# Optimization experiments

Measured on AMD Instinct MI355X. Metric: run time of the kernel, lower is better.

Reference implementation:

```python
import jax, jax.numpy as jnp
import numpy as np

B, F, H, D, TE, CE = 16384, 1024, 64, 256, 4, 4

def setup_inputs() -> dict:
    key = jax.random.key(0)
    ks = iter(jax.random.split(key, 40))
    s = 0.02
    mk = lambda shape: jax.random.normal(next(ks), shape, jnp.float32) * s
    inp = {
        'x_A': jax.random.normal(next(ks), (B, F), jnp.float32),
        'x_S': jax.random.normal(next(ks), (B, F), jnp.float32),
        'x_B': jax.random.normal(next(ks), (B, F), jnp.float32),
        # stacked per-expert weights for the three expert groups (A, Shared, B)
        'W1A': mk((TE, F, H)), 'b1A': mk((TE, H)), 'W2A': mk((TE, H, D)), 'b2A': mk((TE, D)),
        'W1S': mk((CE, F, H)), 'b1S': mk((CE, H)), 'W2S': mk((CE, H, D)), 'b2S': mk((CE, D)),
        'W1B': mk((TE, F, H)), 'b1B': mk((TE, H)), 'W2B': mk((TE, H, D)), 'b2B': mk((TE, D)),
        # gate weights
        'WgA': mk((F, TE + CE)), 'bgA': mk((TE + CE,)),
        'WgB': mk((F, TE + CE)), 'bgB': mk((TE + CE,)),
        'WgS': mk((F, 2 * TE + CE)), 'bgS': mk((2 * TE + CE,)),
    }
    return inp

def _expert_group(x, W1, b1, W2, b2):
    # x: [B,F], W1: [E,F,H] -> [B,E,H]; W2: [E,H,D] -> [B,E,D]
    h = jax.nn.relu(jnp.einsum('bf,efh->beh', x, W1) + b1)  # dropout p=0 -> identity
    return jax.nn.relu(jnp.einsum('beh,ehd->bed', h, W2) + b2)

def reference(x_A, x_S, x_B,
              W1A, b1A, W2A, b2A,
              W1S, b1S, W2S, b2S,
              W1B, b1B, W2B, b2B,
              WgA, bgA, WgB, bgB, WgS, bgS):
    EA = _expert_group(x_A, W1A, b1A, W2A, b2A)  # [B,TE,D]
    ES = _expert_group(x_S, W1S, b1S, W2S, b2S)  # [B,CE,D]
    EB = _expert_group(x_B, W1B, b1B, W2B, b2B)  # [B,TE,D]
    gA = jax.nn.softmax(x_A @ WgA + bgA, axis=1)  # [B,TE+CE]
    gS = jax.nn.softmax(x_S @ WgS + bgS, axis=1)  # [B,2TE+CE]
    gB = jax.nn.softmax(x_B @ WgB + bgB, axis=1)  # [B,TE+CE]
    outA = jnp.einsum('bed,be->bd', jnp.concatenate([EA, ES], axis=1), gA)
    outS = jnp.einsum('bed,be->bd', jnp.concatenate([EA, ES, EB], axis=1), gS)
    outB = jnp.einsum('bed,be->bd', jnp.concatenate([EB, ES], axis=1), gB)
    return (outA, outS, outB)
```

## Files before the change

### kernel.cpp

```cpp
#include <hip/hip_runtime.h>


#define BB 16384
#define FF 1024

typedef _Float16 f16;
typedef __fp16 h16x2 __attribute__((ext_vector_type(2)));
typedef _Float16 f16x8 __attribute__((ext_vector_type(8)));
typedef float f32x4 __attribute__((ext_vector_type(4)));

__device__ __forceinline__ void load_lds16(const void* g, void* l) {
    __builtin_amdgcn_global_load_lds(
        (const __attribute__((address_space(1))) unsigned int*)g,
        (__attribute__((address_space(3))) unsigned int*)l, 16, 0, 0);
}

__device__ __forceinline__ f16x8 pack8(float4 lo, float4 hi) {
    union { f16x8 v; h16x2 p[4]; } u;
    u.p[0] = __builtin_amdgcn_cvt_pkrtz(lo.x, lo.y);
    u.p[1] = __builtin_amdgcn_cvt_pkrtz(lo.z, lo.w);
    u.p[2] = __builtin_amdgcn_cvt_pkrtz(hi.x, hi.y);
    u.p[3] = __builtin_amdgcn_cvt_pkrtz(hi.z, hi.w);
    return u.v;
}

__global__ __launch_bounds__(256) void pack_kernel(
    const float* __restrict__ W1A, const float* __restrict__ W1S, const float* __restrict__ W1B,
    const float* __restrict__ W2A, const float* __restrict__ W2S, const float* __restrict__ W2B,
    const float* __restrict__ WgA, const float* __restrict__ WgS, const float* __restrict__ WgB,
    f16* __restrict__ Wp, f16* __restrict__ W2T, f16* __restrict__ Gp)
{
    int idx = blockIdx.x * 256 + threadIdx.x;
    if (idx < 786432) {
        int g = idx / 262144, rem = idx % 262144;
        int c = rem >> 10, k = rem & 1023;
        const float* W1 = (g == 0) ? W1A : ((g == 1) ? W1S : W1B);
        Wp[idx] = (f16)W1[((c >> 6) << 16) + k * 64 + (c & 63)];
    } else if (idx < 983040) {
        int j = idx - 786432;
        int g = j / 65536, rem = j % 65536;
        int e = rem >> 14, rr = rem & 16383;
        int d = rr >> 6, hh = rr & 63;
        const float* W2 = (g == 0) ? W2A : ((g == 1) ? W2S : W2B);
        W2T[j] = (f16)W2[e * 16384 + hh * 256 + d];
    } else {
        int j = idx - 983040;
        int g = j / 16384, rem = j % 16384;
        int k = rem >> 4, c = rem & 15;
        int ng = (g == 1) ? 12 : 8;
        const float* Wg = (g == 0) ? WgA : ((g == 1) ? WgS : WgB);
        Gp[j] = (c < ng) ? (f16)Wg[k * ng + c] : (f16)0.0f;
    }
}

__global__ __launch_bounds__(256) void l1_kernel(
    const float* __restrict__ xA, const float* __restrict__ xS, const float* __restrict__ xB,
    const float* __restrict__ b1A, const float* __restrict__ b1S, const float* __restrict__ b1B,
    const float* __restrict__ bgA, const float* __restrict__ bgS, const float* __restrict__ bgB,
    const f16* __restrict__ Wp,
    const f16* __restrict__ Gp,
    f16* __restrict__ hbuf,
    float* __restrict__ gates)
{
    const int g = blockIdx.z;
    const float* x  = (g == 0) ? xA  : ((g == 1) ? xS  : xB);
    const float* b1 = (g == 0) ? b1A : ((g == 1) ? b1S : b1B);
    const float* bg = (g == 0) ? bgA : ((g == 1) ? bgS : bgB);
    const int ng = (g == 1) ? 12 : 8;
    float* gout = gates + ((g == 0) ? (size_t)0
                         : (g == 1) ? (size_t)BB * 8
                                    : (size_t)BB * 8 + (size_t)BB * 12);

    const int row0 = blockIdx.y * 128;
    const int col0 = blockIdx.x * 128;
    const bool do_gate = (blockIdx.x == 0);

    __shared__ __align__(16) float Asf[128 * 32];
    __shared__ __align__(16) f16   Bsh[128 * 32];
    __shared__ __align__(16) f16   Gs[16 * 40];

    const int tid  = threadIdx.x;
    const int lane = tid & 63;
    const int wave = tid >> 6;
    const int wm = (wave >> 1) * 64;
    const int wn = (wave & 1) * 64;
    const int lrow = lane & 15;
    const int quad = lane >> 4;

    const f16* Wgrp = Wp + (size_t)g * 256 * 1024;
    const f16* Ggrp = Gp + (size_t)g * 1024 * 16;

    f32x4 acc[4][4] = {};
    f32x4 gacc[4] = {};
    const bool my_gate = do_gate && ((wave & 1) == 0);

    for (int k0 = 0; k0 < FF; k0 += 32) {
#pragma unroll
        for (int r = 0; r < 4; ++r) {
            int s = r * 256 + tid;
            int m = s >> 3, slot = s & 7;
            int seg = slot ^ (m & 7);
            load_lds16(x + (size_t)(row0 + m) * FF + k0 + seg * 4, Asf + s * 4);
        }
#pragma unroll
        for (int r = 0; r < 2; ++r) {
            int s = r * 256 + tid;
            int m = s >> 2, slot = s & 3;
            int seg = slot ^ ((m >> 1) & 3);
            load_lds16(Wgrp + (size_t)(col0 + m) * FF + k0 + seg * 8, Bsh + s * 8);
        }
        if (do_gate) {
#pragma unroll
            for (int r = 0; r < 2; ++r) {
                int idx = r * 256 + tid;
                int k = idx >> 4, c = idx & 15;
                Gs[c * 40 + k] = Ggrp[(size_t)(k0 + k) * 16 + c];
            }
        }
        __syncthreads();

        f16x8 af[4], bfr[4];
#pragma unroll
        for (int i = 0; i < 4; ++i) {
            int m = wm + i * 16 + lrow;
            const float* rp = Asf + m * 32;
            int s0 = (2 * quad) ^ (m & 7);
            int s1 = s0 ^ 1;
            float4 lo = *(const float4*)(rp + s0 * 4);
            float4 hi = *(const float4*)(rp + s1 * 4);
            af[i] = pack8(lo, hi);
        }
#pragma unroll
        for (int j = 0; j < 4; ++j) {
            int n = wn + j * 16 + lrow;
            int slot = quad ^ ((n >> 1) & 3);
            bfr[j] = *(const f16x8*)(Bsh + n * 32 + slot * 8);
        }
#pragma unroll
        for (int i = 0; i < 4; ++i)
#pragma unroll
            for (int j = 0; j < 4; ++j)
                acc[i][j] = __builtin_amdgcn_mfma_f32_16x16x32_f16(af[i], bfr[j], acc[i][j], 0, 0, 0);
        if (my_gate) {
            f16x8 gb = *(const f16x8*)(Gs + lrow * 40 + quad * 8);
#pragma unroll
            for (int i = 0; i < 4; ++i)
                gacc[i] = __builtin_amdgcn_mfma_f32_16x16x32_f16(af[i], gb, gacc[i], 0, 0, 0);
        }
        __syncthreads();
    }

#pragma unroll
    for (int j = 0; j < 4; ++j) {
        int c = col0 + wn + j * 16 + lrow;
        float bias = b1[c];
#pragma unroll
        for (int i = 0; i < 4; ++i) {
#pragma unroll
            for (int r = 0; r < 4; ++r) {
                int row = row0 + wm + i * 16 + quad * 4 + r;
                float v = fmaxf(acc[i][j][r] + bias, 0.0f);
                hbuf[((size_t)g * BB + row) * 256 + c] = (f16)v;
            }
        }
    }

    if (my_gate) {
        int c = lrow;
        bool valid = (c < ng);
        float bias = valid ? bg[c] : 0.0f;
#pragma unroll
        for (int i = 0; i < 4; ++i) {
#pragma unroll
            for (int r = 0; r < 4; ++r) {
                int row = row0 + wm + i * 16 + quad * 4 + r;
                float logit = valid ? (gacc[i][r] + bias) : -1e30f;
                float mx = logit;
#pragma unroll
                for (int m = 1; m < 16; m <<= 1)
                    mx = fmaxf(mx, __shfl_xor(mx, m, 16));
                float ev = valid ? __expf(logit - mx) : 0.0f;
                float sum = ev;
#pragma unroll
                for (int m = 1; m < 16; m <<= 1)
                    sum += __shfl_xor(sum, m, 16);
                if (valid) gout[(size_t)row * ng + c] = ev / sum;
            }
        }
    }
}

__global__ __launch_bounds__(256) void l2_kernel(
    const f16* __restrict__ hbuf,
    const f16* __restrict__ W2T,
    const float* __restrict__ b2A, const float* __restrict__ b2S, const float* __restrict__ b2B,
    const float* __restrict__ gates,
    float* __restrict__ out)
{
    const int o = blockIdx.y;
    const int row0 = blockIdx.x * 64;
    const int tid = threadIdx.x;
    const int lane = tid & 63;
    const int wave = tid >> 6;
    const int wn = wave * 64;
    const int lrow = lane & 15;
    const int quad = lane >> 4;

    const int ng = (o == 1) ? 12 : 8;
    const float* gp = gates + ((o == 0) ? (size_t)0
                             : (o == 1) ? (size_t)BB * 8
                                        : (size_t)BB * 8 + (size_t)BB * 12);

    __shared__ __align__(16) f16 Ash[64 * 64];
    __shared__ __align__(16) f16 Bsh[256 * 64];
    __shared__ float gsh[64 * 12];

    for (int idx = tid; idx < 64 * ng; idx += 256)
        gsh[idx] = gp[(size_t)(row0 + idx / ng) * ng + (idx % ng)];

    f32x4 oacc[4][4] = {};
    const int nc = ng;

    for (int k = 0; k < nc; ++k) {
        int e = k & 3, gc = k, gi;
        if (o == 0)      gi = (k < 4) ? 0 : 1;
        else if (o == 1) gi = k >> 2;
        else             gi = (k < 4) ? 2 : 1;

        const f16* hs = hbuf + ((size_t)gi * BB + row0) * 256 + e * 64;
        const f16* w2 = W2T + (size_t)(gi * 4 + e) * 256 * 64;
        const float* b2 = (gi == 0) ? b2A : ((gi == 1) ? b2S : b2B);

        __syncthreads();
#pragma unroll
        for (int r = 0; r < 2; ++r) {
            int s = r * 256 + tid;
            int m = s >> 3, slot = s & 7;
            int seg = slot ^ (m & 7);
            load_lds16(hs + (size_t)m * 256 + seg * 8, Ash + s * 8);
        }
#pragma unroll
        for (int r = 0; r < 8; ++r) {
            int s = r * 256 + tid;
            int m = s >> 3, slot = s & 7;
            int seg = slot ^ (m & 7);
            load_lds16(w2 + (size_t)m * 64 + seg * 8, Bsh + s * 8);
        }
        __syncthreads();

        f32x4 eacc[4][4] = {};
#pragma unroll
        for (int kk = 0; kk < 2; ++kk) {
            f16x8 af[4], bfr[4];
#pragma unroll
            for (int i = 0; i < 4; ++i) {
                int rr = i * 16 + lrow;
                int slot = (kk * 4 + quad) ^ (rr & 7);
                af[i] = *(const f16x8*)(Ash + rr * 64 + slot * 8);
            }
#pragma unroll
            for (int j = 0; j < 4; ++j) {
                int n = wn + j * 16 + lrow;
                int slot = (kk * 4 + quad) ^ (n & 7);
                bfr[j] = *(const f16x8*)(Bsh + n * 64 + slot * 8);
            }
#pragma unroll
            for (int i = 0; i < 4; ++i)
#pragma unroll
                for (int j = 0; j < 4; ++j)
                    eacc[i][j] = __builtin_amdgcn_mfma_f32_16x16x32_f16(af[i], bfr[j], eacc[i][j], 0, 0, 0);
        }

#pragma unroll
        for (int j = 0; j < 4; ++j) {
            int d = wn + j * 16 + lrow;
            float bias = b2[e * 256 + d];
#pragma unroll
            for (int i = 0; i < 4; ++i) {
#pragma unroll
                for (int r = 0; r < 4; ++r) {
                    int rl = i * 16 + quad * 4 + r;
                    float v = fmaxf(eacc[i][j][r] + bias, 0.0f);
                    oacc[i][j][r] += gsh[rl * ng + gc] * v;
                }
            }
        }
    }

#pragma unroll
    for (int j = 0; j < 4; ++j) {
        int d = wn + j * 16 + lrow;
#pragma unroll
        for (int i = 0; i < 4; ++i) {
#pragma unroll
            for (int r = 0; r < 4; ++r) {
                int rl = i * 16 + quad * 4 + r;
                out[((size_t)o * BB + row0 + rl) * 256 + d] = oacc[i][j][r];
            }
        }
    }
}

extern "C" void kernel_launch(void* const* d_in, const int* in_sizes, int n_in,
                              void* d_out, int out_size, void* d_ws, size_t ws_size,
                              hipStream_t stream)
{
    (void)in_sizes; (void)n_in; (void)out_size; (void)ws_size;

    const float* xA  = (const float*)d_in[0];
    const float* xS  = (const float*)d_in[1];
    const float* xB  = (const float*)d_in[2];
    const float* W1A = (const float*)d_in[3];
    const float* b1A = (const float*)d_in[4];
    const float* W2A = (const float*)d_in[5];
    const float* b2A = (const float*)d_in[6];
    const float* W1S = (const float*)d_in[7];
    const float* b1S = (const float*)d_in[8];
    const float* W2S = (const float*)d_in[9];
    const float* b2S = (const float*)d_in[10];
    const float* W1B = (const float*)d_in[11];
    const float* b1B = (const float*)d_in[12];
    const float* W2B = (const float*)d_in[13];
    const float* b2B = (const float*)d_in[14];
    const float* WgA = (const float*)d_in[15];
    const float* bgA = (const float*)d_in[16];
    const float* WgB = (const float*)d_in[17];
    const float* bgB = (const float*)d_in[18];
    const float* WgS = (const float*)d_in[19];
    const float* bgS = (const float*)d_in[20];

    char* ws = (char*)d_ws;
    f16*   Wp   = (f16*)(ws);
    f16*   W2T  = (f16*)(ws + 0x180000);
    f16*   Gp   = (f16*)(ws + 0x1E0000);
    f16*   hbuf = (f16*)(ws + 0x200000);
    float* gate = (float*)(ws + 0x200000 + 0x1800000);

    pack_kernel<<<4032, 256, 0, stream>>>(W1A, W1S, W1B, W2A, W2S, W2B,
                                          WgA, WgS, WgB, Wp, W2T, Gp);
    l1_kernel<<<dim3(2, 128, 3), 256, 0, stream>>>(
        xA, xS, xB, b1A, b1S, b1B, bgA, bgS, bgB,
        Wp, Gp, hbuf, gate);
    l2_kernel<<<dim3(256, 3), 256, 0, stream>>>(
        hbuf, W2T, b2A, b2S, b2B, gate, (float*)d_out);
}
```

Baseline: 333.6 us.

## Double-buffer LDS tiles in both GEMM kernels to overlap loads with MFMA

Both kernels now keep two LDS buffers. The first kernel prefetches the next K-slice of x, W1 and the gate weights while computing the current one. The second kernel prefetches the next expert's h tile, while the W2 tile stays single-buffered. Synchronisation uses explicit s_waitcnt vmcnt counts and raw s_barrier with sched_barriers, so the asynchronous global-to-LDS copies overlap compute instead of stalling at each __syncthreads. The cost is roughly double the shared memory, which may lower occupancy. The hand-tuned vmcnt values must match the number of outstanding loads exactly, and the gate loads are synchronous register stores mixed into that count.

```diff
diff --git a/kernel.cpp b/kernel.cpp
--- a/kernel.cpp
+++ b/kernel.cpp
@@ -75,9 +75,9 @@
     const int col0 = blockIdx.x * 128;
     const bool do_gate = (blockIdx.x == 0);
 
-    __shared__ __align__(16) float Asf[128 * 32];
-    __shared__ __align__(16) f16   Bsh[128 * 32];
-    __shared__ __align__(16) f16   Gs[16 * 40];
+    __shared__ __align__(16) float Asf[2][128 * 32];
+    __shared__ __align__(16) f16   Bsh[2][128 * 32];
+    __shared__ __align__(16) f16   Gs[2][16 * 40];
 
     const int tid  = threadIdx.x;
     const int lane = tid & 63;
@@ -94,36 +94,58 @@
     f32x4 gacc[4] = {};
     const bool my_gate = do_gate && ((wave & 1) == 0);
 
-    for (int k0 = 0; k0 < FF; k0 += 32) {
+    auto stage_gate = [&](int k0, int buf) {
+        if (do_gate) {
+#pragma unroll
+            for (int r = 0; r < 2; ++r) {
+                int idx = r * 256 + tid;
+                int k = idx >> 4, c = idx & 15;
+                Gs[buf][c * 40 + k] = Ggrp[(size_t)(k0 + k) * 16 + c];
+            }
+        }
+    };
+    auto stage_ab = [&](int k0, int buf) {
 #pragma unroll
         for (int r = 0; r < 4; ++r) {
             int s = r * 256 + tid;
             int m = s >> 3, slot = s & 7;
             int seg = slot ^ (m & 7);
-            load_lds16(x + (size_t)(row0 + m) * FF + k0 + seg * 4, Asf + s * 4);
+            load_lds16(x + (size_t)(row0 + m) * FF + k0 + seg * 4, &Asf[buf][s * 4]);
         }
 #pragma unroll
         for (int r = 0; r < 2; ++r) {
             int s = r * 256 + tid;
             int m = s >> 2, slot = s & 3;
             int seg = slot ^ ((m >> 1) & 3);
-            load_lds16(Wgrp + (size_t)(col0 + m) * FF + k0 + seg * 8, Bsh + s * 8);
-        }
-        if (do_gate) {
-#pragma unroll
-            for (int r = 0; r < 2; ++r) {
-                int idx = r * 256 + tid;
-                int k = idx >> 4, c = idx & 15;
-                Gs[c * 40 + k] = Ggrp[(size_t)(k0 + k) * 16 + c];
-            }
-        }
-        __syncthreads();
+            load_lds16(Wgrp + (size_t)(col0 + m) * FF + k0 + seg * 8, &Bsh[buf][s * 8]);
+        }
+    };
+
+    stage_gate(0, 0);
+    __builtin_amdgcn_sched_barrier(0);
+    stage_ab(0, 0);
+    __builtin_amdgcn_sched_barrier(0);
+
+    for (int t = 0; t < 32; ++t) {
+        const int cur = t & 1;
+        if (t < 31) {
+            stage_gate((t + 1) * 32, cur ^ 1);
+            __builtin_amdgcn_sched_barrier(0);
+            stage_ab((t + 1) * 32, cur ^ 1);
+            __builtin_amdgcn_sched_barrier(0);
+            asm volatile("s_waitcnt vmcnt(6) lgkmcnt(0)" ::: "memory");
+        } else {
+            asm volatile("s_waitcnt vmcnt(0) lgkmcnt(0)" ::: "memory");
+        }
+        __builtin_amdgcn_sched_barrier(0);
+        __builtin_amdgcn_s_barrier();
+        __builtin_amdgcn_sched_barrier(0);
 
         f16x8 af[4], bfr[4];
 #pragma unroll
         for (int i = 0; i < 4; ++i) {
             int m = wm + i * 16 + lrow;
-            const float* rp = Asf + m * 32;
+            const float* rp = &Asf[cur][m * 32];
             int s0 = (2 * quad) ^ (m & 7);
             int s1 = s0 ^ 1;
             float4 lo = *(const float4*)(rp + s0 * 4);
@@ -134,7 +156,7 @@
         for (int j = 0; j < 4; ++j) {
             int n = wn + j * 16 + lrow;
             int slot = quad ^ ((n >> 1) & 3);
-            bfr[j] = *(const f16x8*)(Bsh + n * 32 + slot * 8);
+            bfr[j] = *(const f16x8*)(&Bsh[cur][n * 32 + slot * 8]);
         }
 #pragma unroll
         for (int i = 0; i < 4; ++i)
@@ -142,12 +164,15 @@
             for (int j = 0; j < 4; ++j)
                 acc[i][j] = __builtin_amdgcn_mfma_f32_16x16x32_f16(af[i], bfr[j], acc[i][j], 0, 0, 0);
         if (my_gate) {
-            f16x8 gb = *(const f16x8*)(Gs + lrow * 40 + quad * 8);
+            f16x8 gb = *(const f16x8*)(&Gs[cur][lrow * 40 + quad * 8]);
 #pragma unroll
             for (int i = 0; i < 4; ++i)
                 gacc[i] = __builtin_amdgcn_mfma_f32_16x16x32_f16(af[i], gb, gacc[i], 0, 0, 0);
         }
-        __syncthreads();
+        asm volatile("s_waitcnt lgkmcnt(0)" ::: "memory");
+        __builtin_amdgcn_sched_barrier(0);
+        __builtin_amdgcn_s_barrier();
+        __builtin_amdgcn_sched_barrier(0);
     }
 
 #pragma unroll
@@ -211,42 +236,70 @@
                              : (o == 1) ? (size_t)BB * 8
                                         : (size_t)BB * 8 + (size_t)BB * 12);
 
-    __shared__ __align__(16) f16 Ash[64 * 64];
+    __shared__ __align__(16) f16 Ash[2][64 * 64];
     __shared__ __align__(16) f16 Bsh[256 * 64];
     __shared__ float gsh[64 * 12];
 
-    for (int idx = tid; idx < 64 * ng; idx += 256)
-        gsh[idx] = gp[(size_t)(row0 + idx / ng) * ng + (idx % ng)];
-
-    f32x4 oacc[4][4] = {};
-    const int nc = ng;
-
-    for (int k = 0; k < nc; ++k) {
-        int e = k & 3, gc = k, gi;
-        if (o == 0)      gi = (k < 4) ? 0 : 1;
-        else if (o == 1) gi = k >> 2;
-        else             gi = (k < 4) ? 2 : 1;
-
+    auto group_of = [&](int k) -> int {
+        if (o == 0)      return (k < 4) ? 0 : 1;
+        else if (o == 1) return k >> 2;
+        else             return (k < 4) ? 2 : 1;
+    };
+
+    auto stage_h = [&](int k, int buf) {
+        int gi = group_of(k), e = k & 3;
         const f16* hs = hbuf + ((size_t)gi * BB + row0) * 256 + e * 64;
-        const f16* w2 = W2T + (size_t)(gi * 4 + e) * 256 * 64;
-        const float* b2 = (gi == 0) ? b2A : ((gi == 1) ? b2S : b2B);
-
-        __syncthreads();
 #pragma unroll
         for (int r = 0; r < 2; ++r) {
             int s = r * 256 + tid;
             int m = s >> 3, slot = s & 7;
             int seg = slot ^ (m & 7);
-            load_lds16(hs + (size_t)m * 256 + seg * 8, Ash + s * 8);
-        }
+            load_lds16(hs + (size_t)m * 256 + seg * 8, &Ash[buf][s * 8]);
+        }
+    };
+    auto stage_w2 = [&](int k) {
+        int gi = group_of(k), e = k & 3;
+        const f16* w2 = W2T + (size_t)(gi * 4 + e) * 256 * 64;
 #pragma unroll
         for (int r = 0; r < 8; ++r) {
             int s = r * 256 + tid;
             int m = s >> 3, slot = s & 7;
             int seg = slot ^ (m & 7);
-            load_lds16(w2 + (size_t)m * 64 + seg * 8, Bsh + s * 8);
-        }
-        __syncthreads();
+            load_lds16(w2 + (size_t)m * 64 + seg * 8, &Bsh[s * 8]);
+        }
+    };
+
+    for (int idx = tid; idx < 64 * ng; idx += 256)
+        gsh[idx] = gp[(size_t)(row0 + idx / ng) * ng + (idx % ng)];
+    __builtin_amdgcn_sched_barrier(0);
+    stage_h(0, 0);
+    __builtin_amdgcn_sched_barrier(0);
+
+    f32x4 oacc[4][4] = {};
+
+    for (int k = 0; k < ng; ++k) {
+        const int cur = k & 1;
+        const int gi = group_of(k), e = k & 3;
+        const float* b2 = (gi == 0) ? b2A : ((gi == 1) ? b2S : b2B);
+
+        float bias4[4];
+#pragma unroll
+        for (int j = 0; j < 4; ++j)
+            bias4[j] = b2[e * 256 + wn + j * 16 + lrow];
+        __builtin_amdgcn_sched_barrier(0);
+
+        stage_w2(k);
+        __builtin_amdgcn_sched_barrier(0);
+        if (k + 1 < ng) {
+            stage_h(k + 1, cur ^ 1);
+            __builtin_amdgcn_sched_barrier(0);
+            asm volatile("s_waitcnt vmcnt(2) lgkmcnt(0)" ::: "memory");
+        } else {
+            asm volatile("s_waitcnt vmcnt(0) lgkmcnt(0)" ::: "memory");
+        }
+        __builtin_amdgcn_sched_barrier(0);
+        __builtin_amdgcn_s_barrier();
+        __builtin_amdgcn_sched_barrier(0);
 
         f32x4 eacc[4][4] = {};
 #pragma unroll
@@ -256,13 +309,13 @@
             for (int i = 0; i < 4; ++i) {
                 int rr = i * 16 + lrow;
                 int slot = (kk * 4 + quad) ^ (rr & 7);
-                af[i] = *(const f16x8*)(Ash + rr * 64 + slot * 8);
+                af[i] = *(const f16x8*)(&Ash[cur][rr * 64 + slot * 8]);
             }
 #pragma unroll
             for (int j = 0; j < 4; ++j) {
                 int n = wn + j * 16 + lrow;
                 int slot = (kk * 4 + quad) ^ (n & 7);
-                bfr[j] = *(const f16x8*)(Bsh + n * 64 + slot * 8);
+                bfr[j] = *(const f16x8*)(&Bsh[n * 64 + slot * 8]);
             }
 #pragma unroll
             for (int i = 0; i < 4; ++i)
@@ -273,18 +326,21 @@
 
 #pragma unroll
         for (int j = 0; j < 4; ++j) {
-            int d = wn + j * 16 + lrow;
-            float bias = b2[e * 256 + d];
+            float bias = bias4[j];
 #pragma unroll
             for (int i = 0; i < 4; ++i) {
 #pragma unroll
                 for (int r = 0; r < 4; ++r) {
                     int rl = i * 16 + quad * 4 + r;
                     float v = fmaxf(eacc[i][j][r] + bias, 0.0f);
-                    oacc[i][j][r] += gsh[rl * ng + gc] * v;
+                    oacc[i][j][r] += gsh[rl * ng + k] * v;
                 }
             }
         }
+        asm volatile("s_waitcnt lgkmcnt(0)" ::: "memory");
+        __builtin_amdgcn_sched_barrier(0);
+        __builtin_amdgcn_s_barrier();
+        __builtin_amdgcn_sched_barrier(0);
     }
 
 #pragma unroll
```

New measurement: 348.4 us. +4.5%, slower.
